# Kernel tuning notes

Measured on AMD Instinct MI355X. Metric: run time of the kernel, lower is better.

Reference implementation:

```python
import jax, jax.numpy as jnp
import numpy as np
from jax import lax

B_, DIM, H, W, Dd = 2, 256, 16, 16, 16
DI, N, DTR, K = 256, 8, 16, 4   # d_inner (expand=1), d_state, dt_rank=ceil(256/16), d_conv
OUT_C = 1200
L = H * W * Dd
EPS = 1e-5


def setup_inputs() -> dict:
    key = jax.random.key(0)
    ks = jax.random.split(key, 20)
    g = lambda k, s: jax.random.normal(k, s, jnp.float32) * 0.02
    A_log = jnp.log(jnp.broadcast_to(jnp.arange(1, N + 1, dtype=jnp.float32), (DI, N)))
    dt_bias = jnp.full((DI,), float(np.log(np.expm1(0.01))), jnp.float32)
    return {
        "input0": jax.random.normal(ks[0], (B_, DIM, H, W, Dd), jnp.float32),
        "input1": jax.random.normal(ks[1], (B_, DIM, H, W, Dd), jnp.float32),
        "norm0_w": jnp.ones((DIM,), jnp.float32),
        "norm0_b": jnp.zeros((DIM,), jnp.float32),
        "norm1_w": jnp.ones((DIM,), jnp.float32),
        "norm1_b": jnp.zeros((DIM,), jnp.float32),
        "in_proj_w": g(ks[2], (DI, DIM)),
        "in_projz_w": g(ks[3], (DI, DIM)),
        "conv1d_w": g(ks[4], (DI, 1, K)),
        "conv1d_bias": jnp.zeros((DI,), jnp.float32),
        "conv1db_w": g(ks[5], (DI, 1, K)),
        "conv1db_bias": jnp.zeros((DI,), jnp.float32),
        "xproj_w": g(ks[6], (DTR + 2 * N, DI)),
        "xprojb_w": g(ks[7], (DTR + 2 * N, DI)),
        "dtproj_w": g(ks[8], (DI, DTR)),
        "dtproj_bias": dt_bias,
        "dtprojb_w": g(ks[9], (DI, DTR)),
        "dtprojb_bias": dt_bias,
        "A_log": A_log,
        "Ab_log": A_log,
        "D_p": jnp.ones((DI,), jnp.float32),
        "D_b": jnp.ones((DI,), jnp.float32),
        "rms_w": jnp.ones((DI,), jnp.float32),
        "out_proj_w": g(ks[10], (DIM, DI)),
        "conv3d_w": g(ks[11], (OUT_C, DIM)),
        "conv3d_bias": jnp.zeros((OUT_C,), jnp.float32),
    }


def _layernorm(x, w, b):
    m = x.mean(-1, keepdims=True)
    v = ((x - m) ** 2).mean(-1, keepdims=True)
    return (x - m) * lax.rsqrt(v + EPS) * w + b


def _rmsnorm(x, w):
    return x * lax.rsqrt((x * x).mean(-1, keepdims=True) + EPS) * w


def _ssm_dir(x, z, conv_w, conv_b, xproj_w, dtproj_w, dtproj_bias, A_log, Dp):
    # One direction of the bimamba-v2 selective scan. x, z: (b, L, d_inner)
    xt = x.transpose(0, 2, 1)  # (b, d, L)
    xc = lax.conv_general_dilated(xt, conv_w, (1,), [(K - 1, 0)], feature_group_count=DI)
    x = jax.nn.silu(xc + conv_b[None, :, None]).transpose(0, 2, 1)  # causal dw-conv + silu
    dbl = x @ xproj_w.T                                   # (b, L, dt_rank + 2n)
    dt, Bm, Cm = dbl[..., :DTR], dbl[..., DTR:DTR + N], dbl[..., DTR + N:]
    dt = jax.nn.softplus(dt @ dtproj_w.T + dtproj_bias)    # (b, L, d)
    A = -jnp.exp(A_log)                                    # (d, n)
    dA = jnp.exp(dt[..., None] * A)                        # (b, L, d, n)
    dBu = (dt * x)[..., None] * Bm[:, :, None, :]          # (b, L, d, n)

    def step(h, inp):
        dA_t, dBu_t, C_t = inp
        h = h * dA_t + dBu_t
        return h, jnp.einsum('bdn,bn->bd', h, C_t)

    h0 = jnp.zeros((x.shape[0], DI, N), x.dtype)
    _, ys = lax.scan(step, h0, (dA.transpose(1, 0, 2, 3), dBu.transpose(1, 0, 2, 3), Cm.transpose(1, 0, 2)))
    y = ys.transpose(1, 0, 2) + x * Dp                     # (b, L, d)
    return y * jax.nn.silu(z)                              # gate from the matching branch


def _forward(input0, input1, norm0_w, norm0_b, norm1_w, norm1_b, in_proj_w, in_projz_w,
             conv1d_w, conv1d_bias, conv1db_w, conv1db_bias, xproj_w, xprojb_w,
             dtproj_w, dtproj_bias, dtprojb_w, dtprojb_bias, A_log, Ab_log,
             D_p, D_b, rms_w, out_proj_w, conv3d_w, conv3d_bias):
    b = input0.shape[0]
    skip = input0
    seq0 = input0.transpose(0, 2, 3, 4, 1).reshape(b, L, DIM)  # b (h w d) c
    seq1 = input1.transpose(0, 2, 3, 4, 1).reshape(b, L, DIM)
    seq0 = _layernorm(seq0, norm0_w, norm0_b)
    seq1 = _layernorm(seq1, norm1_w, norm1_b)
    x = seq0 @ in_proj_w.T    # SSM input from input0
    z = seq1 @ in_projz_w.T   # gate from extra_emb (input1)
    y_f = _ssm_dir(x, z, conv1d_w, conv1d_bias, xproj_w, dtproj_w, dtproj_bias, A_log, D_p)
    y_b = _ssm_dir(x[:, ::-1], z[:, ::-1], conv1db_w, conv1db_bias, xprojb_w,
                   dtprojb_w, dtprojb_bias, Ab_log, D_b)[:, ::-1]

    def head(y):
        o = _rmsnorm(y, rms_w) @ out_proj_w.T              # use_norm=True, then out_proj
        o = o.reshape(b, H, W, Dd, DIM).transpose(0, 4, 1, 2, 3) + skip
        return jnp.einsum('bchwd,oc->bohwd', o, conv3d_w) + conv3d_bias[None, :, None, None, None]

    out = head((y_f + y_b) * 0.5)   # if_devide_out=True
    return out, head(y_f), head(y_b)


def reference(input0, input1, norm0_w, norm0_b, norm1_w, norm1_b, in_proj_w, in_projz_w,
              conv1d_w, conv1d_bias, conv1db_w, conv1db_bias, xproj_w, xprojb_w,
              dtproj_w, dtproj_bias, dtprojb_w, dtprojb_bias, A_log, Ab_log,
              D_p, D_b, rms_w, out_proj_w, conv3d_w, conv3d_bias):
    return _forward(input0, input1, norm0_w, norm0_b, norm1_w, norm1_b, in_proj_w, in_projz_w,
                    conv1d_w, conv1d_bias, conv1db_w, conv1db_bias, xproj_w, xprojb_w,
                    dtproj_w, dtproj_bias, dtprojb_w, dtprojb_bias, A_log, Ab_log,
                    D_p, D_b, rms_w, out_proj_w, conv3d_w, conv3d_bias)
```

## Files before the change

kernel.cpp:

```cpp
#include <hip/hip_runtime.h>
#include <cstdint>

#define LTOK 4096
#define NTOK 8192
#define NCH  256
#define CLEN 16

typedef __attribute__((ext_vector_type(4))) float f32x4;
typedef __attribute__((ext_vector_type(8))) short s16x8;

__device__ __forceinline__ short f2bf(float f) {
  union { float f; unsigned u; } x; x.f = f;
  unsigned r = x.u + 0x7FFFu + ((x.u >> 16) & 1u);
  return (short)(r >> 16);
}
__device__ __forceinline__ float bf2f(short s) {
  union { float f; unsigned u; } x;
  x.u = ((unsigned)(unsigned short)s) << 16;
  return x.f;
}
__device__ __forceinline__ void gl_lds16(const void* g, void* l) {
  __builtin_amdgcn_global_load_lds((const unsigned int*)g, (unsigned int*)l, 16, 0, 0);
}

__global__ __launch_bounds__(256) void wconv_k(
    const float* __restrict__ wx, const float* __restrict__ wz,
    const float* __restrict__ wo, const float* __restrict__ wc,
    short* __restrict__ Wx, short* __restrict__ Wz,
    short* __restrict__ Wo, short* __restrict__ Wc)
{
  int idx = blockIdx.x * 256 + threadIdx.x;
  if (idx < 65536)       Wx[idx] = f2bf(wx[idx]);
  else if (idx < 131072) Wz[idx - 65536] = f2bf(wz[idx - 65536]);
  else if (idx < 196608) Wo[idx - 131072] = f2bf(wo[idx - 131072]);
  else {
    int k = idx - 196608;
    int row = k >> 8;
    Wc[k] = (row < 1200) ? f2bf(wc[k]) : (short)0;
  }
}

__global__ __launch_bounds__(256) void ln_transpose_kernel(
    const float* __restrict__ in0, const float* __restrict__ in1,
    const float* __restrict__ w0, const float* __restrict__ b0,
    const float* __restrict__ w1, const float* __restrict__ b1,
    short* __restrict__ xlnz, float* __restrict__ seqT)
{
  __shared__ float tile[32 * 257];
  __shared__ float mu[32], rs[32];
  const int tid = threadIdx.x;
  const int b  = blockIdx.x >> 7;
  const int l0 = (blockIdx.x & 127) << 5;

  for (int pass = 0; pass < 2; ++pass) {
    const float* in = pass ? in1 : in0;
    #pragma unroll 8
    for (int i = 0; i < 32; ++i) {
      int e = (i << 8) + tid;
      int c = e >> 5, lo = e & 31;
      tile[lo * 257 + c] = in[((size_t)(b * 256 + c) << 12) + l0 + lo];
    }
    __syncthreads();
    if (tid < 32) {
      float s = 0.f, ss = 0.f;
      #pragma unroll 8
      for (int c = 0; c < 256; ++c) {
        float v = tile[tid * 257 + c];
        s += v; ss += v * v;
      }
      float m = s * (1.f / 256.f);
      float var = ss * (1.f / 256.f) - m * m;
      mu[tid] = m;
      rs[tid] = rsqrtf(var + 1e-5f);
    }
    __syncthreads();
    const float* w  = pass ? w1 : w0;
    const float* bb = pass ? b1 : b0;
    float wv = w[tid], bv = bb[tid];
    #pragma unroll 8
    for (int i = 0; i < 32; ++i) {
      float v = tile[i * 257 + tid];
      int row = (pass ? 8192 : 0) + (b << 12) + l0 + i;
      xlnz[(size_t)row * 256 + tid] = f2bf((v - mu[i]) * rs[i] * wv + bv);
      if (pass == 0) seqT[(((size_t)b << 12) + l0 + i) * 256 + tid] = v;
    }
    __syncthreads();
  }
}

template <int EPI>
__global__ __launch_bounds__(256) void gemm_fast(
    const short* __restrict__ A, const short* __restrict__ W0,
    const short* __restrict__ W1, float* __restrict__ Cf,
    short* __restrict__ Cb, const float* __restrict__ ADD,
    const float* __restrict__ bias, int Msplit)
{
  __shared__ short As[4096];
  __shared__ short Bs[4096];
  const int tid  = threadIdx.x;
  const int lane = tid & 63, wave = tid >> 6;
  const int m0 = blockIdx.y << 7;
  const int n0 = blockIdx.x << 7;
  const short* W = (EPI == 0 && m0 >= Msplit) ? W1 : W0;

  const int sr = tid >> 2;
  const int sc = (tid & 3) << 3;
  const int mf = lane & 15, kq = lane >> 4;
  const int wm = (wave & 1) << 6, wn = (wave >> 1) << 6;

  const short* Ar0 = A + (size_t)(m0 + sr) * 256 + sc;
  const short* Ar1 = A + (size_t)(m0 + 64 + sr) * 256 + sc;
  const short* Br0 = W + (size_t)(n0 + sr) * 256 + sc;
  const short* Br1 = W + (size_t)(n0 + 64 + sr) * 256 + sc;
  short* AsW = &As[wave << 9];
  short* BsW = &Bs[wave << 9];

  f32x4 acc[4][4] = {};

  for (int kt = 0; kt < 256; kt += 32) {
    gl_lds16(Ar0 + kt, AsW);
    gl_lds16(Ar1 + kt, AsW + 2048);
    gl_lds16(Br0 + kt, BsW);
    gl_lds16(Br1 + kt, BsW + 2048);
    __syncthreads();
    s16x8 af[4], bfr[4];
    #pragma unroll
    for (int i = 0; i < 4; ++i)
      af[i] = *(const s16x8*)&As[((wm + (i << 4) + mf) << 5) + (kq << 3)];
    #pragma unroll
    for (int j = 0; j < 4; ++j)
      bfr[j] = *(const s16x8*)&Bs[((wn + (j << 4) + mf) << 5) + (kq << 3)];
    #pragma unroll
    for (int i = 0; i < 4; ++i)
      #pragma unroll
      for (int j = 0; j < 4; ++j)
        acc[i][j] = __builtin_amdgcn_mfma_f32_16x16x32_bf16(af[i], bfr[j], acc[i][j], 0, 0, 0);
    __syncthreads();
  }

  if (EPI == 0) {
    #pragma unroll
    for (int i = 0; i < 4; ++i) {
      int gm = m0 + wm + (i << 4) + (kq << 2);
      #pragma unroll
      for (int j = 0; j < 4; ++j) {
        int gn = n0 + wn + (j << 4) + mf;
        #pragma unroll
        for (int r = 0; r < 4; ++r)
          Cf[(size_t)(gm + r) * 256 + gn] = acc[i][j][r];
      }
    }
  } else if (EPI == 1) {
    #pragma unroll
    for (int i = 0; i < 4; ++i) {
      int gm = m0 + wm + (i << 4) + (kq << 2);
      #pragma unroll
      for (int j = 0; j < 4; ++j) {
        int gn = n0 + wn + (j << 4) + mf;
        #pragma unroll
        for (int r = 0; r < 4; ++r) {
          int tok = (gm + r) & 8191;
          float v = acc[i][j][r] + ADD[(size_t)tok * 256 + gn];
          Cb[(size_t)(gm + r) * 256 + gn] = f2bf(v);
        }
      }
    }
  } else {
    const int head = m0 >> 13, bb = (m0 >> 12) & 1, lb = m0 & 4095;
    float* obase = Cf + (size_t)head * (2u * 1200u * 4096u) + (size_t)bb * (1200u * 4096u);
    #pragma unroll
    for (int i = 0; i < 4; ++i) {
      int l = lb + wm + (i << 4) + (kq << 2);
      #pragma unroll
      for (int j = 0; j < 4; ++j) {
        int gn = n0 + wn + (j << 4) + mf;
        if (gn < 1200) {
          float bv = bias[gn];
          f32x4 v = acc[i][j];
          v[0] += bv; v[1] += bv; v[2] += bv; v[3] += bv;
          *(f32x4*)&obase[(size_t)gn * 4096 + l] = v;
        }
      }
    }
  }
}

__global__ __launch_bounds__(256) void gemm_small(
    const float* __restrict__ A, const float* __restrict__ W,
    float* __restrict__ C, int N)
{
  __shared__ float smem[2560];
  short* As = (short*)smem;
  short* Bs = ((short*)smem) + 64 * 40;
  const int tid  = threadIdx.x;
  const int lane = tid & 63, wave = tid >> 6;
  const int m0 = blockIdx.y << 6;
  const int n0 = blockIdx.x << 6;
  const int wm = (wave & 1) << 5, wn = (wave >> 1) << 5;
  const int mf = lane & 15;
  const int kq = (lane >> 4) << 3;
  const int rq = (lane >> 4) << 2;
  f32x4 acc[2][2] = {};
  for (int kt = 0; kt < 256; kt += 32) {
    #pragma unroll
    for (int i = 0; i < 8; ++i) {
      int e = (i << 8) + tid;
      int r = e >> 5, c = e & 31;
      As[r * 40 + c] = f2bf(A[(size_t)(m0 + r) * 256 + kt + c]);
      int n = n0 + r;
      Bs[r * 40 + c] = f2bf(n < N ? W[(size_t)n * 256 + kt + c] : 0.f);
    }
    __syncthreads();
    s16x8 af[2], bfr[2];
    #pragma unroll
    for (int i = 0; i < 2; ++i) af[i] = *(const s16x8*)&As[(wm + (i << 4) + mf) * 40 + kq];
    #pragma unroll
    for (int j = 0; j < 2; ++j) bfr[j] = *(const s16x8*)&Bs[(wn + (j << 4) + mf) * 40 + kq];
    #pragma unroll
    for (int i = 0; i < 2; ++i)
      #pragma unroll
      for (int j = 0; j < 2; ++j)
        acc[i][j] = __builtin_amdgcn_mfma_f32_16x16x32_bf16(af[i], bfr[j], acc[i][j], 0, 0, 0);
    __syncthreads();
  }
  #pragma unroll
  for (int i = 0; i < 2; ++i)
    #pragma unroll
    for (int j = 0; j < 2; ++j)
      #pragma unroll
      for (int r = 0; r < 4; ++r) {
        int gm = m0 + wm + (i << 4) + rq + r;
        int gn = n0 + wn + (j << 4) + mf;
        if (gn < N) C[(size_t)gm * N + gn] = acc[i][j][r];
      }
}

template <int REV>
__global__ __launch_bounds__(256) void conv_silu_k(
    const float* __restrict__ x, const float* __restrict__ cw,
    const float* __restrict__ cb, float* __restrict__ xc)
{
  const int d = threadIdx.x;
  const int b = blockIdx.x >> 8;
  const int t0 = (blockIdx.x & 255) << 4;
  const float w0 = cw[(d << 2)], w1 = cw[(d << 2) + 1],
              w2 = cw[(d << 2) + 2], w3 = cw[(d << 2) + 3];
  const float bias = cb[d];
  const size_t xb = ((size_t)b) << 12;
  float h0 = 0.f, h1 = 0.f, h2 = 0.f;
  #pragma unroll
  for (int i = 0; i < 3; ++i) {
    int ts = t0 - 3 + i;
    float v = 0.f;
    if (ts >= 0) { int tn = REV ? 4095 - ts : ts; v = x[(xb + tn) * 256 + d]; }
    h0 = h1; h1 = h2; h2 = v;
  }
  for (int s = 0; s < 16; ++s) {
    int ts = t0 + s;
    int tn = REV ? 4095 - ts : ts;
    float xv = x[(xb + tn) * 256 + d];
    float a = bias + w0 * h0 + w1 * h1 + w2 * h2 + w3 * xv;
    h0 = h1; h1 = h2; h2 = xv;
    xc[(xb + ts) * 256 + d] = a / (1.f + __expf(-a));
  }
}

__global__ __launch_bounds__(256) void scan_p1(
    const float* __restrict__ xc, const float* __restrict__ dbl,
    const float* __restrict__ dtw, const float* __restrict__ dtb,
    const float* __restrict__ A_log, float* __restrict__ P, float* __restrict__ Q)
{
  __shared__ float dl[512];
  const int d = threadIdx.x;
  const int b = blockIdx.x >> 8, ch = blockIdx.x & 255;
  const int tok0 = (b << 12) + (ch << 4);
  dl[d]       = dbl[(size_t)tok0 * 32 + d];
  dl[256 + d] = dbl[(size_t)tok0 * 32 + 256 + d];
  float wrow[16];
  #pragma unroll
  for (int r = 0; r < 16; ++r) wrow[r] = dtw[(d << 4) + r];
  const float bias = dtb[d];
  float Av[8], p[8], q[8];
  #pragma unroll
  for (int n = 0; n < 8; ++n) { Av[n] = -expf(A_log[(d << 3) + n]); p[n] = 1.f; q[n] = 0.f; }
  __syncthreads();
  for (int s = 0; s < 16; ++s) {
    float a = bias;
    #pragma unroll
    for (int r = 0; r < 16; ++r) a = fmaf(dl[(s << 5) + r], wrow[r], a);
    float dtv = (a > 20.f) ? a : log1pf(__expf(a));
    size_t tok = (size_t)tok0 + s;
    float xv = xc[tok * 256 + d];
    float du = dtv * xv;
    #pragma unroll
    for (int n = 0; n < 8; ++n) {
      float dA = __expf(dtv * Av[n]);
      p[n] *= dA;
      q[n] = fmaf(q[n], dA, du * dl[(s << 5) + 16 + n]);
    }
  }
  size_t ob = ((size_t)((b << 8) + ch) * 8) * 256 + d;
  #pragma unroll
  for (int n = 0; n < 8; ++n) { P[ob + (n << 8)] = p[n]; Q[ob + (n << 8)] = q[n]; }
}

__global__ __launch_bounds__(256) void scan_p2a(
    const float* __restrict__ P, const float* __restrict__ Q,
    float* __restrict__ SP, float* __restrict__ SQ)
{
  const int d = threadIdx.x;
  const int bidx = blockIdx.x;
  const int b = bidx >> 7, n = (bidx >> 4) & 7, sup = bidx & 15;
  float sp = 1.f, sq = 0.f;
  #pragma unroll 4
  for (int c = 0; c < 16; ++c) {
    int ch = (sup << 4) + c;
    size_t idx = ((size_t)((b << 8) + ch) * 8 + n) * 256 + d;
    float pp = P[idx], qq = Q[idx];
    sq = fmaf(pp, sq, qq);
    sp *= pp;
  }
  size_t o2 = ((size_t)(((b << 3) + n) << 4) + sup) * 256 + d;
  SP[o2] = sp; SQ[o2] = sq;
}

__global__ __launch_bounds__(256) void scan_p2b(
    const float* __restrict__ SP, const float* __restrict__ SQ, float* __restrict__ SH)
{
  const int d = threadIdx.x;
  const int bn = blockIdx.x;
  float h = 0.f;
  #pragma unroll 4
  for (int sup = 0; sup < 16; ++sup) {
    size_t i = ((size_t)(bn << 4) + sup) * 256 + d;
    SH[i] = h;
    h = fmaf(SP[i], h, SQ[i]);
  }
}

__global__ __launch_bounds__(256) void scan_p2c(
    const float* __restrict__ P, const float* __restrict__ Q,
    const float* __restrict__ SH, float* __restrict__ Hs)
{
  const int d = threadIdx.x;
  const int bidx = blockIdx.x;
  const int b = bidx >> 7, n = (bidx >> 4) & 7, sup = bidx & 15;
  float h = SH[((size_t)(((b << 3) + n) << 4) + sup) * 256 + d];
  #pragma unroll 4
  for (int c = 0; c < 16; ++c) {
    int ch = (sup << 4) + c;
    size_t idx = ((size_t)((b << 8) + ch) * 8 + n) * 256 + d;
    Hs[idx] = h;
    h = fmaf(P[idx], h, Q[idx]);
  }
}

template <int REV>
__global__ __launch_bounds__(256) void scan_p3(
    const float* __restrict__ xc, const float* __restrict__ dbl,
    const float* __restrict__ dtw, const float* __restrict__ dtb,
    const float* __restrict__ Hs, const float* __restrict__ z,
    const float* __restrict__ A_log, const float* __restrict__ Dp,
    short* __restrict__ y)
{
  __shared__ float dl[512];
  const int d = threadIdx.x;
  const int b = blockIdx.x >> 8, ch = blockIdx.x & 255;
  const int tok0 = (b << 12) + (ch << 4);
  dl[d]       = dbl[(size_t)tok0 * 32 + d];
  dl[256 + d] = dbl[(size_t)tok0 * 32 + 256 + d];
  float wrow[16];
  #pragma unroll
  for (int r = 0; r < 16; ++r) wrow[r] = dtw[(d << 4) + r];
  const float bias = dtb[d];
  float Av[8], h[8];
  #pragma unroll
  for (int n = 0; n < 8; ++n) Av[n] = -expf(A_log[(d << 3) + n]);
  size_t hb = ((size_t)((b << 8) + ch) * 8) * 256 + d;
  #pragma unroll
  for (int n = 0; n < 8; ++n) h[n] = Hs[hb + (n << 8)];
  const float Dv = Dp[d];
  __syncthreads();
  for (int s = 0; s < 16; ++s) {
    float a = bias;
    #pragma unroll
    for (int r = 0; r < 16; ++r) a = fmaf(dl[(s << 5) + r], wrow[r], a);
    float dtv = (a > 20.f) ? a : log1pf(__expf(a));
    size_t tok = (size_t)tok0 + s;
    float xv = xc[tok * 256 + d];
    float du = dtv * xv;
    float yv = 0.f;
    #pragma unroll
    for (int n = 0; n < 8; ++n) {
      float dA = __expf(dtv * Av[n]);
      h[n] = fmaf(h[n], dA, du * dl[(s << 5) + 16 + n]);
      yv = fmaf(h[n], dl[(s << 5) + 24 + n], yv);
    }
    yv = fmaf(xv, Dv, yv);
    int t = (int)(tok & 4095);
    int tn = REV ? (4095 - t) : t;
    size_t zi = (((size_t)b << 12) + tn) * 256 + d;
    float zv = z[zi];
    y[zi] = f2bf(yv * zv / (1.f + __expf(-zv)));
  }
}

__global__ __launch_bounds__(256) void rms_all(
    const short* __restrict__ yf, const short* __restrict__ yb,
    const float* __restrict__ w, short* __restrict__ yn)
{
  const int d = threadIdx.x;
  const int mode = blockIdx.y;
  const size_t tok = blockIdx.x;
  size_t i = tok * 256 + d;
  float v;
  if (mode == 0)      v = 0.5f * (bf2f(yf[i]) + bf2f(yb[i]));
  else if (mode == 1) v = bf2f(yf[i]);
  else                v = bf2f(yb[i]);
  float ss = v * v;
  #pragma unroll
  for (int o = 32; o > 0; o >>= 1) ss += __shfl_xor(ss, o, 64);
  __shared__ float red[4];
  if ((d & 63) == 0) red[d >> 6] = ss;
  __syncthreads();
  float tot = red[0] + red[1] + red[2] + red[3];
  float sc = rsqrtf(tot * (1.f / 256.f) + 1e-5f);
  yn[((size_t)mode * 8192 + tok) * 256 + d] = f2bf(v * sc * w[d]);
}

extern "C" void kernel_launch(void* const* d_in, const int* in_sizes, int n_in,
                              void* d_out, int out_size, void* d_ws, size_t ws_size,
                              hipStream_t stream) {
  const float* in0        = (const float*)d_in[0];
  const float* in1        = (const float*)d_in[1];
  const float* n0w        = (const float*)d_in[2];
  const float* n0b        = (const float*)d_in[3];
  const float* n1w        = (const float*)d_in[4];
  const float* n1b        = (const float*)d_in[5];
  const float* in_proj_w  = (const float*)d_in[6];
  const float* in_projz_w = (const float*)d_in[7];
  const float* conv1d_w   = (const float*)d_in[8];
  const float* conv1d_b   = (const float*)d_in[9];
  const float* conv1db_w  = (const float*)d_in[10];
  const float* conv1db_b  = (const float*)d_in[11];
  const float* xproj_w    = (const float*)d_in[12];
  const float* xprojb_w   = (const float*)d_in[13];
  const float* dtproj_w   = (const float*)d_in[14];
  const float* dtproj_b   = (const float*)d_in[15];
  const float* dtprojb_w  = (const float*)d_in[16];
  const float* dtprojb_b  = (const float*)d_in[17];
  const float* A_log      = (const float*)d_in[18];
  const float* Ab_log     = (const float*)d_in[19];
  const float* D_p        = (const float*)d_in[20];
  const float* D_b        = (const float*)d_in[21];
  const float* rms_w      = (const float*)d_in[22];
  const float* out_proj_w = (const float*)d_in[23];
  const float* conv3d_w   = (const float*)d_in[24];
  const float* conv3d_b   = (const float*)d_in[25];
  (void)in_sizes; (void)n_in; (void)out_size; (void)ws_size;

  float* ws = (float*)d_ws;
  size_t o = 0;
  short* xlnz = (short*)(ws + o); o += 2097152;
  float* seqT = ws + o;           o += 2097152;
  float* x    = ws + o;           o += 2097152;
  float* z    = ws + o;           o += 2097152;
  float* xc   = ws + o;           o += 2097152;
  float* dbl  = ws + o;           o += 262144;
  float* P    = ws + o;           o += 1048576;
  float* Q    = ws + o;           o += 1048576;
  float* Hs   = ws + o;           o += 1048576;
  float* SP   = ws + o;           o += 65536;
  float* SQ   = ws + o;           o += 65536;
  float* SH   = ws + o;           o += 65536;
  short* yfb  = (short*)(ws + o); o += 1048576;
  short* ybb  = (short*)(ws + o); o += 1048576;
  short* yn   = (short*)(ws + o); o += 3145728;
  short* obuf = (short*)(ws + o); o += 3145728;
  short* Wx   = (short*)(ws + o); o += 32768;
  short* Wz   = (short*)(ws + o); o += 32768;
  short* Wo   = (short*)(ws + o); o += 32768;
  short* Wc   = (short*)(ws + o); o += 163840;
  float* out  = (float*)d_out;

  dim3 blk(256);

  wconv_k<<<dim3(2048), blk, 0, stream>>>(in_proj_w, in_projz_w, out_proj_w, conv3d_w, Wx, Wz, Wo, Wc);
  ln_transpose_kernel<<<dim3(256), blk, 0, stream>>>(in0, in1, n0w, n0b, n1w, n1b, xlnz, seqT);

  gemm_fast<0><<<dim3(2, 128), blk, 0, stream>>>(xlnz, Wx, Wz, x, nullptr, nullptr, nullptr, 8192);

  conv_silu_k<0><<<dim3(512), blk, 0, stream>>>(x, conv1d_w, conv1d_b, xc);
  gemm_small<<<dim3(1, 128), blk, 0, stream>>>(xc, xproj_w, dbl, 32);
  scan_p1<<<dim3(512), blk, 0, stream>>>(xc, dbl, dtproj_w, dtproj_b, A_log, P, Q);
  scan_p2a<<<dim3(256), blk, 0, stream>>>(P, Q, SP, SQ);
  scan_p2b<<<dim3(16), blk, 0, stream>>>(SP, SQ, SH);
  scan_p2c<<<dim3(256), blk, 0, stream>>>(P, Q, SH, Hs);
  scan_p3<0><<<dim3(512), blk, 0, stream>>>(xc, dbl, dtproj_w, dtproj_b, Hs, z, A_log, D_p, yfb);

  conv_silu_k<1><<<dim3(512), blk, 0, stream>>>(x, conv1db_w, conv1db_b, xc);
  gemm_small<<<dim3(1, 128), blk, 0, stream>>>(xc, xprojb_w, dbl, 32);
  scan_p1<<<dim3(512), blk, 0, stream>>>(xc, dbl, dtprojb_w, dtprojb_b, Ab_log, P, Q);
  scan_p2a<<<dim3(256), blk, 0, stream>>>(P, Q, SP, SQ);
  scan_p2b<<<dim3(16), blk, 0, stream>>>(SP, SQ, SH);
  scan_p2c<<<dim3(256), blk, 0, stream>>>(P, Q, SH, Hs);
  scan_p3<1><<<dim3(512), blk, 0, stream>>>(xc, dbl, dtprojb_w, dtprojb_b, Hs, z, Ab_log, D_b, ybb);

  rms_all<<<dim3(8192, 3), blk, 0, stream>>>(yfb, ybb, rms_w, yn);
  gemm_fast<1><<<dim3(2, 192), blk, 0, stream>>>(yn, Wo, nullptr, nullptr, obuf, seqT, nullptr, 0);
  gemm_fast<2><<<dim3(10, 192), blk, 0, stream>>>(obuf, Wc, nullptr, out, nullptr, nullptr, conv3d_b, 0);
}
```

Measured before the change: 403.0 us.

## Fuse conv, x-proj and scan phase 1 per chunk; batch both directions

```diff
diff --git a/kernel.cpp b/kernel.cpp
--- a/kernel.cpp
+++ b/kernel.cpp
@@ -1,10 +1,7 @@
 #include <hip/hip_runtime.h>
 #include <cstdint>
 
-#define LTOK 4096
 #define NTOK 8192
-#define NCH  256
-#define CLEN 16
 
 typedef __attribute__((ext_vector_type(4))) float f32x4;
 typedef __attribute__((ext_vector_type(8))) short s16x8;
@@ -23,27 +20,14 @@
   __builtin_amdgcn_global_load_lds((const unsigned int*)g, (unsigned int*)l, 16, 0, 0);
 }
 
-__global__ __launch_bounds__(256) void wconv_k(
-    const float* __restrict__ wx, const float* __restrict__ wz,
-    const float* __restrict__ wo, const float* __restrict__ wc,
-    short* __restrict__ Wx, short* __restrict__ Wz,
-    short* __restrict__ Wo, short* __restrict__ Wc)
-{
-  int idx = blockIdx.x * 256 + threadIdx.x;
-  if (idx < 65536)       Wx[idx] = f2bf(wx[idx]);
-  else if (idx < 131072) Wz[idx - 65536] = f2bf(wz[idx - 65536]);
-  else if (idx < 196608) Wo[idx - 131072] = f2bf(wo[idx - 131072]);
-  else {
-    int k = idx - 196608;
-    int row = k >> 8;
-    Wc[k] = (row < 1200) ? f2bf(wc[k]) : (short)0;
-  }
-}
-
 __global__ __launch_bounds__(256) void ln_transpose_kernel(
     const float* __restrict__ in0, const float* __restrict__ in1,
     const float* __restrict__ w0, const float* __restrict__ b0,
     const float* __restrict__ w1, const float* __restrict__ b1,
+    const float* __restrict__ wxp, const float* __restrict__ wzp,
+    const float* __restrict__ wop, const float* __restrict__ wcp,
+    short* __restrict__ Wx, short* __restrict__ Wz,
+    short* __restrict__ Wo, short* __restrict__ Wc,
     short* __restrict__ xlnz, float* __restrict__ seqT)
 {
   __shared__ float tile[32 * 257];
@@ -51,6 +35,21 @@
   const int tid = threadIdx.x;
   const int b  = blockIdx.x >> 7;
   const int l0 = (blockIdx.x & 127) << 5;
+
+  {
+    int base = (int)blockIdx.x << 11;
+    #pragma unroll
+    for (int i = 0; i < 8; ++i) {
+      int idx = base + (i << 8) + tid;
+      if (idx < 65536)       Wx[idx] = f2bf(wxp[idx]);
+      else if (idx < 131072) Wz[idx - 65536] = f2bf(wzp[idx - 65536]);
+      else if (idx < 196608) Wo[idx - 131072] = f2bf(wop[idx - 131072]);
+      else {
+        int k = idx - 196608;
+        Wc[k] = ((k >> 8) < 1200) ? f2bf(wcp[k]) : (short)0;
+      }
+    }
+  }
 
   for (int pass = 0; pass < 2; ++pass) {
     const float* in = pass ? in1 : in0;
@@ -61,17 +60,21 @@
       tile[lo * 257 + c] = in[((size_t)(b * 256 + c) << 12) + l0 + lo];
     }
     __syncthreads();
-    if (tid < 32) {
+    if (tid < 64) {
+      int r = tid & 31, h = tid >> 5;
       float s = 0.f, ss = 0.f;
-      #pragma unroll 8
-      for (int c = 0; c < 256; ++c) {
-        float v = tile[tid * 257 + c];
+      #pragma unroll 16
+      for (int c = h * 128; c < h * 128 + 128; ++c) {
+        float v = tile[r * 257 + c];
         s += v; ss += v * v;
       }
-      float m = s * (1.f / 256.f);
-      float var = ss * (1.f / 256.f) - m * m;
-      mu[tid] = m;
-      rs[tid] = rsqrtf(var + 1e-5f);
+      s  += __shfl_xor(s, 32, 64);
+      ss += __shfl_xor(ss, 32, 64);
+      if (h == 0) {
+        float m = s * (1.f / 256.f);
+        mu[r] = m;
+        rs[r] = rsqrtf(ss * (1.f / 256.f) - m * m + 1e-5f);
+      }
     }
     __syncthreads();
     const float* w  = pass ? w1 : w0;
@@ -178,205 +181,170 @@
           float bv = bias[gn];
           f32x4 v = acc[i][j];
           v[0] += bv; v[1] += bv; v[2] += bv; v[3] += bv;
-          *(f32x4*)&obase[(size_t)gn * 4096 + l] = v;
+          __builtin_nontemporal_store(v, (f32x4*)&obase[(size_t)gn * 4096 + l]);
         }
       }
     }
   }
 }
 
-__global__ __launch_bounds__(256) void gemm_small(
-    const float* __restrict__ A, const float* __restrict__ W,
-    float* __restrict__ C, int N)
-{
-  __shared__ float smem[2560];
-  short* As = (short*)smem;
-  short* Bs = ((short*)smem) + 64 * 40;
-  const int tid  = threadIdx.x;
-  const int lane = tid & 63, wave = tid >> 6;
-  const int m0 = blockIdx.y << 6;
-  const int n0 = blockIdx.x << 6;
-  const int wm = (wave & 1) << 5, wn = (wave >> 1) << 5;
-  const int mf = lane & 15;
-  const int kq = (lane >> 4) << 3;
-  const int rq = (lane >> 4) << 2;
-  f32x4 acc[2][2] = {};
-  for (int kt = 0; kt < 256; kt += 32) {
-    #pragma unroll
-    for (int i = 0; i < 8; ++i) {
-      int e = (i << 8) + tid;
-      int r = e >> 5, c = e & 31;
-      As[r * 40 + c] = f2bf(A[(size_t)(m0 + r) * 256 + kt + c]);
-      int n = n0 + r;
-      Bs[r * 40 + c] = f2bf(n < N ? W[(size_t)n * 256 + kt + c] : 0.f);
-    }
-    __syncthreads();
-    s16x8 af[2], bfr[2];
-    #pragma unroll
-    for (int i = 0; i < 2; ++i) af[i] = *(const s16x8*)&As[(wm + (i << 4) + mf) * 40 + kq];
-    #pragma unroll
-    for (int j = 0; j < 2; ++j) bfr[j] = *(const s16x8*)&Bs[(wn + (j << 4) + mf) * 40 + kq];
-    #pragma unroll
-    for (int i = 0; i < 2; ++i)
-      #pragma unroll
-      for (int j = 0; j < 2; ++j)
-        acc[i][j] = __builtin_amdgcn_mfma_f32_16x16x32_bf16(af[i], bfr[j], acc[i][j], 0, 0, 0);
-    __syncthreads();
+__global__ __launch_bounds__(256) void fused_front(
+    const float* __restrict__ x,
+    const float* __restrict__ cw0, const float* __restrict__ cb0,
+    const float* __restrict__ cw1, const float* __restrict__ cb1,
+    const float* __restrict__ xw0, const float* __restrict__ xw1,
+    const float* __restrict__ dtw0, const float* __restrict__ dtb0,
+    const float* __restrict__ dtw1, const float* __restrict__ dtb1,
+    const float* __restrict__ Alog0, const float* __restrict__ Alog1,
+    float* __restrict__ xcg, float* __restrict__ dblg,
+    float* __restrict__ P, float* __restrict__ Q)
+{
+  __shared__ float xcs[16 * 256];
+  __shared__ short wxs[256 * 33];
+  __shared__ float dls[512];
+  const int tid = threadIdx.x;
+  const int dir = blockIdx.x >> 9;
+  const int b   = (blockIdx.x >> 8) & 1;
+  const int ch  = blockIdx.x & 255;
+  const int t0  = ch << 4;
+  const float* cw   = dir ? cw1 : cw0;
+  const float* cb   = dir ? cb1 : cb0;
+  const float* xw   = dir ? xw1 : xw0;
+  const float* dtw  = dir ? dtw1 : dtw0;
+  const float* dtb  = dir ? dtb1 : dtb0;
+  const float* Alog = dir ? Alog1 : Alog0;
+  const size_t dS = (size_t)dir * (NTOK * 256);
+  const size_t xb = ((size_t)b) << 12;
+
+  {
+    const int d = tid;
+    const float w0 = cw[(d << 2)], w1 = cw[(d << 2) + 1],
+                w2 = cw[(d << 2) + 2], w3 = cw[(d << 2) + 3];
+    const float bias = cb[d];
+    float h0 = 0.f, h1 = 0.f, h2 = 0.f;
+    #pragma unroll
+    for (int i = 0; i < 3; ++i) {
+      int ts = t0 - 3 + i; float v = 0.f;
+      if (ts >= 0) { int tn = dir ? 4095 - ts : ts; v = x[(xb + tn) * 256 + d]; }
+      h0 = h1; h1 = h2; h2 = v;
+    }
+    #pragma unroll
+    for (int s = 0; s < 16; ++s) {
+      int ts = t0 + s;
+      int tn = dir ? 4095 - ts : ts;
+      float xv = x[(xb + tn) * 256 + d];
+      float a = bias + w0 * h0 + w1 * h1 + w2 * h2 + w3 * xv;
+      h0 = h1; h1 = h2; h2 = xv;
+      float v = a / (1.f + __expf(-a));
+      xcs[s * 256 + d] = v;
+      xcg[dS + (xb + ts) * 256 + d] = v;
+    }
   }
   #pragma unroll
-  for (int i = 0; i < 2; ++i)
-    #pragma unroll
-    for (int j = 0; j < 2; ++j)
-      #pragma unroll
-      for (int r = 0; r < 4; ++r) {
-        int gm = m0 + wm + (i << 4) + rq + r;
-        int gn = n0 + wn + (j << 4) + mf;
-        if (gn < N) C[(size_t)gm * N + gn] = acc[i][j][r];
-      }
-}
-
-template <int REV>
-__global__ __launch_bounds__(256) void conv_silu_k(
-    const float* __restrict__ x, const float* __restrict__ cw,
-    const float* __restrict__ cb, float* __restrict__ xc)
+  for (int i = 0; i < 32; ++i) {
+    int flat = (i << 8) + tid;
+    wxs[(flat & 255) * 33 + (flat >> 8)] = f2bf(xw[flat]);
+  }
+  __syncthreads();
+
+  {
+    const int j = tid & 31, s0 = tid >> 5;
+    float a0 = 0.f, a1 = 0.f;
+    #pragma unroll 8
+    for (int r = 0; r < 256; ++r) {
+      float w = bf2f(wxs[r * 33 + j]);
+      a0 = fmaf(xcs[s0 * 256 + r], w, a0);
+      a1 = fmaf(xcs[(s0 + 8) * 256 + r], w, a1);
+    }
+    dls[(s0 << 5) + j] = a0;
+    dls[((s0 + 8) << 5) + j] = a1;
+    size_t db = (size_t)dir * 262144 + ((xb + t0) << 5);
+    dblg[db + tid] = a0;
+    dblg[db + 256 + tid] = a1;
+  }
+  __syncthreads();
+
+  {
+    const int d = tid;
+    float wrow[16];
+    #pragma unroll
+    for (int r = 0; r < 16; ++r) wrow[r] = dtw[(d << 4) + r];
+    const float bias = dtb[d];
+    float Av[8], p[8], q[8];
+    #pragma unroll
+    for (int n = 0; n < 8; ++n) {
+      Av[n] = -expf(Alog[(d << 3) + n]); p[n] = 1.f; q[n] = 0.f;
+    }
+    for (int s = 0; s < 16; ++s) {
+      float a = bias;
+      #pragma unroll
+      for (int r = 0; r < 16; ++r) a = fmaf(dls[(s << 5) + r], wrow[r], a);
+      float dtv = (a > 20.f) ? a : log1pf(__expf(a));
+      float xv = xcs[s * 256 + d];
+      float du = dtv * xv;
+      #pragma unroll
+      for (int n = 0; n < 8; ++n) {
+        float dA = __expf(dtv * Av[n]);
+        p[n] *= dA;
+        q[n] = fmaf(q[n], dA, du * dls[(s << 5) + 16 + n]);
+      }
+    }
+    size_t ob = (size_t)dir * 1048576 + ((size_t)((b << 8) + ch) * 8) * 256 + d;
+    #pragma unroll
+    for (int n = 0; n < 8; ++n) { P[ob + (n << 8)] = p[n]; Q[ob + (n << 8)] = q[n]; }
+  }
+}
+
+__global__ __launch_bounds__(256) void scan_p2(
+    const float* __restrict__ P, const float* __restrict__ Q, float* __restrict__ Hs)
 {
   const int d = threadIdx.x;
-  const int b = blockIdx.x >> 8;
-  const int t0 = (blockIdx.x & 255) << 4;
-  const float w0 = cw[(d << 2)], w1 = cw[(d << 2) + 1],
-              w2 = cw[(d << 2) + 2], w3 = cw[(d << 2) + 3];
-  const float bias = cb[d];
-  const size_t xb = ((size_t)b) << 12;
-  float h0 = 0.f, h1 = 0.f, h2 = 0.f;
-  #pragma unroll
-  for (int i = 0; i < 3; ++i) {
-    int ts = t0 - 3 + i;
-    float v = 0.f;
-    if (ts >= 0) { int tn = REV ? 4095 - ts : ts; v = x[(xb + tn) * 256 + d]; }
-    h0 = h1; h1 = h2; h2 = v;
-  }
-  for (int s = 0; s < 16; ++s) {
-    int ts = t0 + s;
-    int tn = REV ? 4095 - ts : ts;
-    float xv = x[(xb + tn) * 256 + d];
-    float a = bias + w0 * h0 + w1 * h1 + w2 * h2 + w3 * xv;
-    h0 = h1; h1 = h2; h2 = xv;
-    xc[(xb + ts) * 256 + d] = a / (1.f + __expf(-a));
-  }
-}
-
-__global__ __launch_bounds__(256) void scan_p1(
-    const float* __restrict__ xc, const float* __restrict__ dbl,
-    const float* __restrict__ dtw, const float* __restrict__ dtb,
-    const float* __restrict__ A_log, float* __restrict__ P, float* __restrict__ Q)
+  const int bid = blockIdx.x;
+  const int dir = bid >> 4, b = (bid >> 3) & 1, n = bid & 7;
+  const size_t dOff = (size_t)dir * 1048576;
+  float h = 0.f;
+  #pragma unroll 8
+  for (int ch = 0; ch < 256; ++ch) {
+    size_t i = dOff + ((size_t)((b << 8) + ch) * 8 + n) * 256 + d;
+    Hs[i] = h;
+    h = fmaf(P[i], h, Q[i]);
+  }
+}
+
+__global__ __launch_bounds__(256) void scan_p3(
+    const float* __restrict__ xcg, const float* __restrict__ dblg,
+    const float* __restrict__ dtw0, const float* __restrict__ dtb0,
+    const float* __restrict__ dtw1, const float* __restrict__ dtb1,
+    const float* __restrict__ Hs, const float* __restrict__ z,
+    const float* __restrict__ Alog0, const float* __restrict__ Alog1,
+    const float* __restrict__ Dp0, const float* __restrict__ Dp1,
+    short* __restrict__ yall)
 {
   __shared__ float dl[512];
   const int d = threadIdx.x;
-  const int b = blockIdx.x >> 8, ch = blockIdx.x & 255;
-  const int tok0 = (b << 12) + (ch << 4);
-  dl[d]       = dbl[(size_t)tok0 * 32 + d];
-  dl[256 + d] = dbl[(size_t)tok0 * 32 + 256 + d];
-  float wrow[16];
-  #pragma unroll
-  for (int r = 0; r < 16; ++r) wrow[r] = dtw[(d << 4) + r];
-  const float bias = dtb[d];
-  float Av[8], p[8], q[8];
-  #pragma unroll
-  for (int n = 0; n < 8; ++n) { Av[n] = -expf(A_log[(d << 3) + n]); p[n] = 1.f; q[n] = 0.f; }
-  __syncthreads();
-  for (int s = 0; s < 16; ++s) {
-    float a = bias;
-    #pragma unroll
-    for (int r = 0; r < 16; ++r) a = fmaf(dl[(s << 5) + r], wrow[r], a);
-    float dtv = (a > 20.f) ? a : log1pf(__expf(a));
-    size_t tok = (size_t)tok0 + s;
-    float xv = xc[tok * 256 + d];
-    float du = dtv * xv;
-    #pragma unroll
-    for (int n = 0; n < 8; ++n) {
-      float dA = __expf(dtv * Av[n]);
-      p[n] *= dA;
-      q[n] = fmaf(q[n], dA, du * dl[(s << 5) + 16 + n]);
-    }
-  }
-  size_t ob = ((size_t)((b << 8) + ch) * 8) * 256 + d;
-  #pragma unroll
-  for (int n = 0; n < 8; ++n) { P[ob + (n << 8)] = p[n]; Q[ob + (n << 8)] = q[n]; }
-}
-
-__global__ __launch_bounds__(256) void scan_p2a(
-    const float* __restrict__ P, const float* __restrict__ Q,
-    float* __restrict__ SP, float* __restrict__ SQ)
-{
-  const int d = threadIdx.x;
-  const int bidx = blockIdx.x;
-  const int b = bidx >> 7, n = (bidx >> 4) & 7, sup = bidx & 15;
-  float sp = 1.f, sq = 0.f;
-  #pragma unroll 4
-  for (int c = 0; c < 16; ++c) {
-    int ch = (sup << 4) + c;
-    size_t idx = ((size_t)((b << 8) + ch) * 8 + n) * 256 + d;
-    float pp = P[idx], qq = Q[idx];
-    sq = fmaf(pp, sq, qq);
-    sp *= pp;
-  }
-  size_t o2 = ((size_t)(((b << 3) + n) << 4) + sup) * 256 + d;
-  SP[o2] = sp; SQ[o2] = sq;
-}
-
-__global__ __launch_bounds__(256) void scan_p2b(
-    const float* __restrict__ SP, const float* __restrict__ SQ, float* __restrict__ SH)
-{
-  const int d = threadIdx.x;
-  const int bn = blockIdx.x;
-  float h = 0.f;
-  #pragma unroll 4
-  for (int sup = 0; sup < 16; ++sup) {
-    size_t i = ((size_t)(bn << 4) + sup) * 256 + d;
-    SH[i] = h;
-    h = fmaf(SP[i], h, SQ[i]);
-  }
-}
-
-__global__ __launch_bounds__(256) void scan_p2c(
-    const float* __restrict__ P, const float* __restrict__ Q,
-    const float* __restrict__ SH, float* __restrict__ Hs)
-{
-  const int d = threadIdx.x;
-  const int bidx = blockIdx.x;
-  const int b = bidx >> 7, n = (bidx >> 4) & 7, sup = bidx & 15;
-  float h = SH[((size_t)(((b << 3) + n) << 4) + sup) * 256 + d];
-  #pragma unroll 4
-  for (int c = 0; c < 16; ++c) {
-    int ch = (sup << 4) + c;
-    size_t idx = ((size_t)((b << 8) + ch) * 8 + n) * 256 + d;
-    Hs[idx] = h;
-    h = fmaf(P[idx], h, Q[idx]);
-  }
-}
-
-template <int REV>
-__global__ __launch_bounds__(256) void scan_p3(
-    const float* __restrict__ xc, const float* __restrict__ dbl,
-    const float* __restrict__ dtw, const float* __restrict__ dtb,
-    const float* __restrict__ Hs, const float* __restrict__ z,
-    const float* __restrict__ A_log, const float* __restrict__ Dp,
-    short* __restrict__ y)
-{
-  __shared__ float dl[512];
-  const int d = threadIdx.x;
-  const int b = blockIdx.x >> 8, ch = blockIdx.x & 255;
-  const int tok0 = (b << 12) + (ch << 4);
-  dl[d]       = dbl[(size_t)tok0 * 32 + d];
-  dl[256 + d] = dbl[(size_t)tok0 * 32 + 256 + d];
+  const int dir = blockIdx.x >> 9;
+  const int b   = (blockIdx.x >> 8) & 1;
+  const int ch  = blockIdx.x & 255;
+  const int t0  = ch << 4;
+  const float* dtw  = dir ? dtw1 : dtw0;
+  const float* dtb  = dir ? dtb1 : dtb0;
+  const float* Alog = dir ? Alog1 : Alog0;
+  const float* Dp   = dir ? Dp1 : Dp0;
+  const size_t dS = (size_t)dir * (NTOK * 256);
+  const size_t xb = ((size_t)b) << 12;
+  short* y = yall + (size_t)dir * (NTOK * 256);
+
+  size_t db = (size_t)dir * 262144 + ((xb + t0) << 5);
+  dl[d]       = dblg[db + d];
+  dl[256 + d] = dblg[db + 256 + d];
   float wrow[16];
   #pragma unroll
   for (int r = 0; r < 16; ++r) wrow[r] = dtw[(d << 4) + r];
   const float bias = dtb[d];
   float Av[8], h[8];
   #pragma unroll
-  for (int n = 0; n < 8; ++n) Av[n] = -expf(A_log[(d << 3) + n]);
-  size_t hb = ((size_t)((b << 8) + ch) * 8) * 256 + d;
+  for (int n = 0; n < 8; ++n) Av[n] = -expf(Alog[(d << 3) + n]);
+  size_t hb = (size_t)dir * 1048576 + ((size_t)((b << 8) + ch) * 8) * 256 + d;
   #pragma unroll
   for (int n = 0; n < 8; ++n) h[n] = Hs[hb + (n << 8)];
   const float Dv = Dp[d];
@@ -386,8 +354,8 @@
     #pragma unroll
     for (int r = 0; r < 16; ++r) a = fmaf(dl[(s << 5) + r], wrow[r], a);
     float dtv = (a > 20.f) ? a : log1pf(__expf(a));
-    size_t tok = (size_t)tok0 + s;
-    float xv = xc[tok * 256 + d];
+    int ts = t0 + s;
+    float xv = xcg[dS + (xb + ts) * 256 + d];
     float du = dtv * xv;
     float yv = 0.f;
     #pragma unroll
@@ -397,9 +365,8 @@
       yv = fmaf(h[n], dl[(s << 5) + 24 + n], yv);
     }
     yv = fmaf(xv, Dv, yv);
-    int t = (int)(tok & 4095);
-    int tn = REV ? (4095 - t) : t;
-    size_t zi = (((size_t)b << 12) + tn) * 256 + d;
+    int tn = dir ? (4095 - ts) : ts;
+    size_t zi = (xb + tn) * 256 + d;
     float zv = z[zi];
     y[zi] = f2bf(yv * zv / (1.f + __expf(-zv)));
   }
@@ -465,16 +432,12 @@
   float* seqT = ws + o;           o += 2097152;
   float* x    = ws + o;           o += 2097152;
   float* z    = ws + o;           o += 2097152;
-  float* xc   = ws + o;           o += 2097152;
-  float* dbl  = ws + o;           o += 262144;
-  float* P    = ws + o;           o += 1048576;
-  float* Q    = ws + o;           o += 1048576;
-  float* Hs   = ws + o;           o += 1048576;
-  float* SP   = ws + o;           o += 65536;
-  float* SQ   = ws + o;           o += 65536;
-  float* SH   = ws + o;           o += 65536;
-  short* yfb  = (short*)(ws + o); o += 1048576;
-  short* ybb  = (short*)(ws + o); o += 1048576;
+  float* xc2  = ws + o;           o += 4194304;
+  float* dbl2 = ws + o;           o += 524288;
+  float* P    = ws + o;           o += 2097152;
+  float* Q    = ws + o;           o += 2097152;
+  float* Hs   = ws + o;           o += 2097152;
+  short* yall = (short*)(ws + o); o += 2097152;
   short* yn   = (short*)(ws + o); o += 3145728;
   short* obuf = (short*)(ws + o); o += 3145728;
   short* Wx   = (short*)(ws + o); o += 32768;
@@ -485,28 +448,25 @@
 
   dim3 blk(256);
 
-  wconv_k<<<dim3(2048), blk, 0, stream>>>(in_proj_w, in_projz_w, out_proj_w, conv3d_w, Wx, Wz, Wo, Wc);
-  ln_transpose_kernel<<<dim3(256), blk, 0, stream>>>(in0, in1, n0w, n0b, n1w, n1b, xlnz, seqT);
+  ln_transpose_kernel<<<dim3(256), blk, 0, stream>>>(
+      in0, in1, n0w, n0b, n1w, n1b,
+      in_proj_w, in_projz_w, out_proj_w, conv3d_w, Wx, Wz, Wo, Wc,
+      xlnz, seqT);
 
   gemm_fast<0><<<dim3(2, 128), blk, 0, stream>>>(xlnz, Wx, Wz, x, nullptr, nullptr, nullptr, 8192);
 
-  conv_silu_k<0><<<dim3(512), blk, 0, stream>>>(x, conv1d_w, conv1d_b, xc);
-  gemm_small<<<dim3(1, 128), blk, 0, stream>>>(xc, xproj_w, dbl, 32);
-  scan_p1<<<dim3(512), blk, 0, stream>>>(xc, dbl, dtproj_w, dtproj_b, A_log, P, Q);
-  scan_p2a<<<dim3(256), blk, 0, stream>>>(P, Q, SP, SQ);
-  scan_p2b<<<dim3(16), blk, 0, stream>>>(SP, SQ, SH);
-  scan_p2c<<<dim3(256), blk, 0, stream>>>(P, Q, SH, Hs);
-  scan_p3<0><<<dim3(512), blk, 0, stream>>>(xc, dbl, dtproj_w, dtproj_b, Hs, z, A_log, D_p, yfb);
-
-  conv_silu_k<1><<<dim3(512), blk, 0, stream>>>(x, conv1db_w, conv1db_b, xc);
-  gemm_small<<<dim3(1, 128), blk, 0, stream>>>(xc, xprojb_w, dbl, 32);
-  scan_p1<<<dim3(512), blk, 0, stream>>>(xc, dbl, dtprojb_w, dtprojb_b, Ab_log, P, Q);
-  scan_p2a<<<dim3(256), blk, 0, stream>>>(P, Q, SP, SQ);
-  scan_p2b<<<dim3(16), blk, 0, stream>>>(SP, SQ, SH);
-  scan_p2c<<<dim3(256), blk, 0, stream>>>(P, Q, SH, Hs);
-  scan_p3<1><<<dim3(512), blk, 0, stream>>>(xc, dbl, dtprojb_w, dtprojb_b, Hs, z, Ab_log, D_b, ybb);
-
-  rms_all<<<dim3(8192, 3), blk, 0, stream>>>(yfb, ybb, rms_w, yn);
+  fused_front<<<dim3(1024), blk, 0, stream>>>(
+      x, conv1d_w, conv1d_b, conv1db_w, conv1db_b,
+      xproj_w, xprojb_w, dtproj_w, dtproj_b, dtprojb_w, dtprojb_b,
+      A_log, Ab_log, xc2, dbl2, P, Q);
+
+  scan_p2<<<dim3(32), blk, 0, stream>>>(P, Q, Hs);
+
+  scan_p3<<<dim3(1024), blk, 0, stream>>>(
+      xc2, dbl2, dtproj_w, dtproj_b, dtprojb_w, dtprojb_b,
+      Hs, z, A_log, Ab_log, D_p, D_b, yall);
+
+  rms_all<<<dim3(8192, 3), blk, 0, stream>>>(yall, yall + 2097152, rms_w, yn);
   gemm_fast<1><<<dim3(2, 192), blk, 0, stream>>>(yn, Wo, nullptr, nullptr, obuf, seqT, nullptr, 0);
   gemm_fast<2><<<dim3(10, 192), blk, 0, stream>>>(obuf, Wc, nullptr, out, nullptr, nullptr, conv3d_b, 0);
 }
```

New measurement: 339.0 us. 1.19x faster.
